# Kernel optimization log

Hardware: AMD Instinct MI355X
Metric: run time of the kernel (lower is better)

Reference implementation:

```python
import jax, jax.numpy as jnp
import numpy as np

WS = 7  # window size
NH = 8  # num heads


def _relative_position_index(ws):
    coords = np.stack(np.meshgrid(np.arange(ws), np.arange(ws), indexing='ij'), axis=0)
    flat = coords.reshape(2, -1)                       # [2, ws*ws]
    rel = flat[:, :, None] - flat[:, None, :]          # [2, N, N]
    rel = rel.transpose(1, 2, 0)                       # [N, N, 2]
    xx = (rel[:, :, 0] + ws - 1) * (2 * ws - 1)
    yy = rel[:, :, 1] + ws - 1
    return jnp.asarray(xx + yy, dtype=jnp.int32)       # [N, N]


def setup_inputs() -> dict:
    key = jax.random.key(0)
    ks = jax.random.split(key, 6)
    B_, N, C = 4096, WS * WS, 256
    return {
        'x': jax.random.normal(ks[0], (B_, N, C), dtype=jnp.float32),
        'qkv_w': jax.random.normal(ks[1], (C, 3 * C), dtype=jnp.float32) * 0.02,
        'qkv_b': jax.random.normal(ks[2], (3 * C,), dtype=jnp.float32) * 0.02,
        'rpb_table': jax.random.normal(ks[3], ((2 * WS - 1) ** 2, NH), dtype=jnp.float32) * 0.02,
        'proj_w': jax.random.normal(ks[4], (C, C), dtype=jnp.float32) * 0.02,
        'proj_b': jax.random.normal(ks[5], (C,), dtype=jnp.float32) * 0.02,
    }


def reference(x, qkv_w, qkv_b, rpb_table, proj_w, proj_b):
    B_, N, C = x.shape
    D = C // NH
    scale = D ** -0.5
    rpi = _relative_position_index(WS)                  # [N, N] int

    qkv = x @ qkv_w + qkv_b                             # [B, N, 3C]
    qkv = qkv.reshape(B_, N, 3, NH, D).transpose(2, 0, 3, 1, 4)
    q, k, v = qkv[0], qkv[1], qkv[2]                    # each [B, H, N, D]

    attn = jnp.einsum('bhnd,bhmd->bhnm', q * scale, k)  # [B, H, N, N]
    bias = rpb_table[rpi.reshape(-1)].reshape(N, N, NH).transpose(2, 0, 1)
    attn = jax.nn.softmax(attn + bias[None], axis=-1)

    out = jnp.einsum('bhnm,bhmd->bhnd', attn, v)        # [B, H, N, D]
    out = out.transpose(0, 2, 1, 3).reshape(B_, N, C)
    return out @ proj_w + proj_b
```

## Files before the change

### kernel.cpp

```cpp
#include <hip/hip_runtime.h>
#include <stdint.h>


typedef __attribute__((ext_vector_type(8))) short bf16x8;
typedef __attribute__((ext_vector_type(4))) float f32x4;

__device__ __forceinline__ unsigned short f2bf(float f) {
    unsigned u = __float_as_uint(f);
    u += 0x7fffu + ((u >> 16) & 1u);
    return (unsigned short)(u >> 16);
}
__device__ __forceinline__ unsigned pk2(float a, float b) {
    return (unsigned)f2bf(a) | ((unsigned)f2bf(b) << 16);
}

__global__ void k_prep(const float* __restrict__ qkv_w, const float* __restrict__ proj_w,
                       short* __restrict__ Wqkv_t, short* __restrict__ Wproj_t) {
    int tid = blockIdx.x * 256 + threadIdx.x;
    if (tid < 196608) {
        int nn = tid >> 8, kk = tid & 255;
        Wqkv_t[tid] = (short)f2bf(qkv_w[kk * 768 + nn]);
    } else {
        int t2 = tid - 196608;
        int nn = t2 >> 8, kk = t2 & 255;
        Wproj_t[t2] = (short)f2bf(proj_w[kk * 256 + nn]);
    }
}

#define XS_OFF 0
#define QS_OFF 16384
#define KS_OFF 32768
#define VT_OFF 49152
#define PL_OFF 67584

__global__ __launch_bounds__(512, 1) void k_fused(
        const float* __restrict__ x, const short* __restrict__ Wq,
        const short* __restrict__ Wp, const float* __restrict__ qkv_b,
        const float* __restrict__ rpb, const float* __restrict__ proj_b,
        float* __restrict__ out) {
    __shared__ __align__(16) short smem[76800];
    __shared__ float rpbs[1352];

    const int b = blockIdx.x;
    const int t = threadIdx.x;
    const int w = t >> 6, lane = t & 63;
    const int l15 = lane & 15, g = lane >> 4;
    const int cs8 = (l15 >> 1) & 3;
    const int swz = (g ^ cs8) << 3;

    f32x4 zero = {0.f, 0.f, 0.f, 0.f};

    for (int i = t; i < 1352; i += 512) rpbs[i] = rpb[i];
    #pragma unroll
    for (int i = 0; i < 4; i++) {
        int cid = t + i * 512;
        int tok = cid >> 5, c = cid & 31;
        uint4 w4 = make_uint4(0u, 0u, 0u, 0u);
        if (tok < 49) {
            const float4* s = (const float4*)(x + ((size_t)b * 49 + tok) * 256 + c * 8);
            float4 f0 = s[0], f1 = s[1];
            w4 = make_uint4(pk2(f0.x, f0.y), pk2(f0.z, f0.w),
                            pk2(f1.x, f1.y), pk2(f1.z, f1.w));
        }
        *(uint4*)&smem[XS_OFF + tok * 256 + ((c ^ (tok & 7)) << 3)] = w4;
    }
    __syncthreads();

    {
        f32x4 acc[6][4];
        #pragma unroll
        for (int i = 0; i < 6; i++)
            #pragma unroll
            for (int j = 0; j < 4; j++) acc[i][j] = zero;

        const short* wbase = Wq + (size_t)(w * 32 + l15) * 256 + g * 8;
        #pragma unroll
        for (int ks = 0; ks < 8; ks++) {
            bf16x8 af[6], bfj[4];
            #pragma unroll
            for (int p = 0; p < 3; p++)
                #pragma unroll
                for (int it = 0; it < 2; it++)
                    af[p * 2 + it] = *(const bf16x8*)(wbase + p * 65536 + it * 4096 + ks * 32);
            int xsl = (((ks << 2) + g) ^ (l15 & 7)) << 3;
            #pragma unroll
            for (int j = 0; j < 4; j++)
                bfj[j] = *(const bf16x8*)&smem[XS_OFF + (j * 16 + l15) * 256 + xsl];
            #pragma unroll
            for (int i = 0; i < 6; i++)
                #pragma unroll
                for (int j = 0; j < 4; j++)
                    acc[i][j] = __builtin_amdgcn_mfma_f32_16x16x32_bf16(
                        af[i], bfj[j], acc[i][j], 0, 0, 0);
        }
        #pragma unroll
        for (int p = 0; p < 2; p++) {
            int base = (p ? KS_OFF : QS_OFF) + w * 2048;
            #pragma unroll
            for (int it = 0; it < 2; it++) {
                int d0 = it * 16 + g * 4;
                float4 bv = *(const float4*)&qkv_b[p * 256 + w * 32 + d0];
                #pragma unroll
                for (int j = 0; j < 4; j++) {
                    int tok = j * 16 + l15;
                    f32x4 a = acc[p * 2 + it][j];
                    unsigned* dst = (unsigned*)&smem[base + tok * 32 +
                                                     (((d0 >> 3) ^ cs8) << 3) + (d0 & 7)];
                    dst[0] = pk2(a[0] + bv.x, a[1] + bv.y);
                    dst[1] = pk2(a[2] + bv.z, a[3] + bv.w);
                }
            }
        }
        {
            short* vt = &smem[VT_OFF + w * 2304];
            #pragma unroll
            for (int it = 0; it < 2; it++) {
                int d0 = it * 16 + g * 4;
                float4 bv = *(const float4*)&qkv_b[512 + w * 32 + d0];
                #pragma unroll
                for (int j = 0; j < 4; j++) {
                    int tok = j * 16 + l15;
                    f32x4 a = acc[4 + it][j];
                    vt[(d0 + 0) * 72 + tok] = (short)f2bf(a[0] + bv.x);
                    vt[(d0 + 1) * 72 + tok] = (short)f2bf(a[1] + bv.y);
                    vt[(d0 + 2) * 72 + tok] = (short)f2bf(a[2] + bv.z);
                    vt[(d0 + 3) * 72 + tok] = (short)f2bf(a[3] + bv.w);
                }
            }
        }
    }

    {
        const int h = w;
        const short* Kb = &smem[KS_OFF + h * 2048];
        const short* Qb = &smem[QS_OFF + h * 2048];
        bf16x8 ka[4], qb4[4], va[2][2];
        #pragma unroll
        for (int mt = 0; mt < 4; mt++)
            ka[mt] = *(const bf16x8*)&Kb[(mt * 16 + l15) * 32 + swz];
        #pragma unroll
        for (int nt = 0; nt < 4; nt++)
            qb4[nt] = *(const bf16x8*)&Qb[(nt * 16 + l15) * 32 + swz];
        #pragma unroll
        for (int dt = 0; dt < 2; dt++)
            #pragma unroll
            for (int kk = 0; kk < 2; kk++)
                va[dt][kk] = *(const bf16x8*)&smem[VT_OFF + h * 2304 +
                                                  (dt * 16 + l15) * 72 + kk * 32 + g * 8];
        short* Plw = &smem[PL_OFF + w * 1152];
        short* AOw = &smem[QS_OFF + h * 2048];
        const float scale = 0.17677669529663687f;

        #pragma unroll
        for (int nt = 0; nt < 4; nt++) {
            f32x4 s4[4];
            #pragma unroll
            for (int mt = 0; mt < 4; mt++)
                s4[mt] = __builtin_amdgcn_mfma_f32_16x16x32_bf16(ka[mt], qb4[nt], zero, 0, 0, 0);
            int n = nt * 16 + l15;
            int ni = n / 7;
            int an = 13 * ni + (n - 7 * ni) + 84;
            #pragma unroll
            for (int mt = 0; mt < 4; mt++)
                #pragma unroll
                for (int r = 0; r < 4; r++) {
                    int m = mt * 16 + g * 4 + r;
                    int mi = m / 7;
                    int idx = an - (13 * mi + (m - 7 * mi));
                    idx = idx < 0 ? 0 : (idx > 168 ? 168 : idx);
                    float val = s4[mt][r] * scale + rpbs[idx * 8 + h];
                    s4[mt][r] = (m < 49) ? val : -1e30f;
                }
            float tmax = -1e30f;
            #pragma unroll
            for (int mt = 0; mt < 4; mt++)
                #pragma unroll
                for (int r = 0; r < 4; r++) tmax = fmaxf(tmax, s4[mt][r]);
            tmax = fmaxf(tmax, __shfl_xor(tmax, 16));
            tmax = fmaxf(tmax, __shfl_xor(tmax, 32));
            float rsum = 0.f;
            #pragma unroll
            for (int mt = 0; mt < 4; mt++)
                #pragma unroll
                for (int r = 0; r < 4; r++) {
                    float e = __expf(s4[mt][r] - tmax);
                    s4[mt][r] = e;
                    rsum += e;
                }
            rsum += __shfl_xor(rsum, 16);
            rsum += __shfl_xor(rsum, 32);

            #pragma unroll
            for (int mt = 0; mt < 4; mt++) {
                unsigned* dst = (unsigned*)&Plw[l15 * 72 + mt * 16 + g * 4];
                dst[0] = pk2(s4[mt][0], s4[mt][1]);
                dst[1] = pk2(s4[mt][2], s4[mt][3]);
            }
            bf16x8 pb0 = *(const bf16x8*)&Plw[l15 * 72 + g * 8];
            bf16x8 pb1 = *(const bf16x8*)&Plw[l15 * 72 + 32 + g * 8];
            f32x4 o0 = __builtin_amdgcn_mfma_f32_16x16x32_bf16(va[0][0], pb0, zero, 0, 0, 0);
            o0 = __builtin_amdgcn_mfma_f32_16x16x32_bf16(va[0][1], pb1, o0, 0, 0, 0);
            f32x4 o1 = __builtin_amdgcn_mfma_f32_16x16x32_bf16(va[1][0], pb0, zero, 0, 0, 0);
            o1 = __builtin_amdgcn_mfma_f32_16x16x32_bf16(va[1][1], pb1, o1, 0, 0, 0);
            float inv = 1.f / rsum;
            {
                int d0 = g * 4;
                unsigned* dst = (unsigned*)&AOw[n * 32 + (((d0 >> 3) ^ cs8) << 3) + (d0 & 7)];
                dst[0] = pk2(o0[0] * inv, o0[1] * inv);
                dst[1] = pk2(o0[2] * inv, o0[3] * inv);
            }
            {
                int d0 = 16 + g * 4;
                unsigned* dst = (unsigned*)&AOw[n * 32 + (((d0 >> 3) ^ cs8) << 3) + (d0 & 7)];
                dst[0] = pk2(o1[0] * inv, o1[1] * inv);
                dst[1] = pk2(o1[2] * inv, o1[3] * inv);
            }
        }
    }
    __syncthreads();

    {
        f32x4 acc2[2][4];
        #pragma unroll
        for (int i = 0; i < 2; i++)
            #pragma unroll
            for (int j = 0; j < 4; j++) acc2[i][j] = zero;

        const short* pbase = Wp + (size_t)(w * 32 + l15) * 256 + g * 8;
        #pragma unroll
        for (int ks = 0; ks < 8; ks++) {
            bf16x8 af2[2], bf2[4];
            af2[0] = *(const bf16x8*)(pbase + ks * 32);
            af2[1] = *(const bf16x8*)(pbase + 4096 + ks * 32);
            #pragma unroll
            for (int j = 0; j < 4; j++)
                bf2[j] = *(const bf16x8*)&smem[QS_OFF + ks * 2048 + (j * 16 + l15) * 32 + swz];
            #pragma unroll
            for (int i = 0; i < 2; i++)
                #pragma unroll
                for (int j = 0; j < 4; j++)
                    acc2[i][j] = __builtin_amdgcn_mfma_f32_16x16x32_bf16(
                        af2[i], bf2[j], acc2[i][j], 0, 0, 0);
        }
        #pragma unroll
        for (int it = 0; it < 2; it++) {
            int fo = w * 32 + it * 16 + g * 4;
            float4 bv = *(const float4*)&proj_b[fo];
            #pragma unroll
            for (int j = 0; j < 4; j++) {
                int tok = j * 16 + l15;
                if (tok < 49) {
                    f32x4 a = acc2[it][j];
                    float4 val = make_float4(a[0] + bv.x, a[1] + bv.y,
                                             a[2] + bv.z, a[3] + bv.w);
                    *(float4*)&out[((size_t)b * 49 + tok) * 256 + fo] = val;
                }
            }
        }
    }
}

extern "C" void kernel_launch(void* const* d_in, const int* in_sizes, int n_in,
                              void* d_out, int out_size, void* d_ws, size_t ws_size,
                              hipStream_t stream) {
    const float* x      = (const float*)d_in[0];
    const float* qkv_w  = (const float*)d_in[1];
    const float* qkv_b  = (const float*)d_in[2];
    const float* rpb    = (const float*)d_in[3];
    const float* proj_w = (const float*)d_in[4];
    const float* proj_b = (const float*)d_in[5];
    float* out = (float*)d_out;

    short* Wqkv_t  = (short*)d_ws;
    short* Wproj_t = Wqkv_t + 768 * 256;
    if (ws_size < 524288ull) return;

    k_prep<<<1024, 256, 0, stream>>>(qkv_w, proj_w, Wqkv_t, Wproj_t);
    k_fused<<<4096, 512, 0, stream>>>(x, Wqkv_t, Wproj_t, qkv_b, rpb, proj_b, out);
}
```

Before: 679.9 us.

## Shrink shared memory via per-wave staging buffers to raise block occupancy

Replaces the separate Q, K, V-transpose and P shared-memory regions with one per-wave scratch area. Q, then K, then V are written into it one after another and loaded into registers, and the attention output reuses the x buffer. This cuts LDS use from about 153KB to about 70KB per block so more than one block can share a CU, and the launch bound now asks for 4 blocks per CU. The bias table is also transposed so each head reads its own contiguous slice. The cost is that the 96-float accumulator stays live into the attention phase, and the tighter launch bound caps registers. Together these raise the risk of heavy register spilling.

After: 1.130 ms. 66.2% more time.

```diff
diff --git a/kernel.cpp b/kernel.cpp
--- a/kernel.cpp
+++ b/kernel.cpp
@@ -28,17 +28,15 @@
 }
 
 #define XS_OFF 0
-#define QS_OFF 16384
-#define KS_OFF 32768
-#define VT_OFF 49152
-#define PL_OFF 67584
-
-__global__ __launch_bounds__(512, 1) void k_fused(
+#define AO_OFF 0
+#define SW_OFF 16384
+
+__global__ __launch_bounds__(512, 4) void k_fused(
         const float* __restrict__ x, const short* __restrict__ Wq,
         const short* __restrict__ Wp, const float* __restrict__ qkv_b,
         const float* __restrict__ rpb, const float* __restrict__ proj_b,
         float* __restrict__ out) {
-    __shared__ __align__(16) short smem[76800];
+    __shared__ __align__(16) short smem[34816];
     __shared__ float rpbs[1352];
 
     const int b = blockIdx.x;
@@ -50,7 +48,7 @@
 
     f32x4 zero = {0.f, 0.f, 0.f, 0.f};
 
-    for (int i = t; i < 1352; i += 512) rpbs[i] = rpb[i];
+    for (int i = t; i < 1352; i += 512) rpbs[(i & 7) * 169 + (i >> 3)] = rpb[i];
     #pragma unroll
     for (int i = 0; i < 4; i++) {
         int cid = t + i * 512;
@@ -66,13 +64,12 @@
     }
     __syncthreads();
 
+    f32x4 acc[6][4];
+    #pragma unroll
+    for (int i = 0; i < 6; i++)
+        #pragma unroll
+        for (int j = 0; j < 4; j++) acc[i][j] = zero;
     {
-        f32x4 acc[6][4];
-        #pragma unroll
-        for (int i = 0; i < 6; i++)
-            #pragma unroll
-            for (int j = 0; j < 4; j++) acc[i][j] = zero;
-
         const short* wbase = Wq + (size_t)(w * 32 + l15) * 256 + g * 8;
         #pragma unroll
         for (int ks = 0; ks < 8; ks++) {
@@ -93,62 +90,74 @@
                     acc[i][j] = __builtin_amdgcn_mfma_f32_16x16x32_bf16(
                         af[i], bfj[j], acc[i][j], 0, 0, 0);
         }
-        #pragma unroll
-        for (int p = 0; p < 2; p++) {
-            int base = (p ? KS_OFF : QS_OFF) + w * 2048;
-            #pragma unroll
-            for (int it = 0; it < 2; it++) {
-                int d0 = it * 16 + g * 4;
-                float4 bv = *(const float4*)&qkv_b[p * 256 + w * 32 + d0];
-                #pragma unroll
-                for (int j = 0; j < 4; j++) {
-                    int tok = j * 16 + l15;
-                    f32x4 a = acc[p * 2 + it][j];
-                    unsigned* dst = (unsigned*)&smem[base + tok * 32 +
-                                                     (((d0 >> 3) ^ cs8) << 3) + (d0 & 7)];
-                    dst[0] = pk2(a[0] + bv.x, a[1] + bv.y);
-                    dst[1] = pk2(a[2] + bv.z, a[3] + bv.w);
-                }
-            }
-        }
-        {
-            short* vt = &smem[VT_OFF + w * 2304];
-            #pragma unroll
-            for (int it = 0; it < 2; it++) {
-                int d0 = it * 16 + g * 4;
-                float4 bv = *(const float4*)&qkv_b[512 + w * 32 + d0];
-                #pragma unroll
-                for (int j = 0; j < 4; j++) {
-                    int tok = j * 16 + l15;
-                    f32x4 a = acc[4 + it][j];
-                    vt[(d0 + 0) * 72 + tok] = (short)f2bf(a[0] + bv.x);
-                    vt[(d0 + 1) * 72 + tok] = (short)f2bf(a[1] + bv.y);
-                    vt[(d0 + 2) * 72 + tok] = (short)f2bf(a[2] + bv.z);
-                    vt[(d0 + 3) * 72 + tok] = (short)f2bf(a[3] + bv.w);
-                }
-            }
-        }
-    }
+    }
+    __syncthreads();
 
     {
         const int h = w;
-        const short* Kb = &smem[KS_OFF + h * 2048];
-        const short* Qb = &smem[QS_OFF + h * 2048];
-        bf16x8 ka[4], qb4[4], va[2][2];
+        short* SW = &smem[SW_OFF + w * 2304];
+        const int d0a = g * 4;
+        const int d0b = 16 + g * 4;
+        const int sda = (((d0a >> 3) ^ cs8) << 3) + (d0a & 7);
+        const int sdb = (((d0b >> 3) ^ cs8) << 3) + (d0b & 7);
+
+        bf16x8 qb4[4], ka[4], va[2][2];
+
+        #pragma unroll
+        for (int it = 0; it < 2; it++) {
+            float4 bv = *(const float4*)&qkv_b[w * 32 + it * 16 + d0a];
+            int sd = it ? sdb : sda;
+            #pragma unroll
+            for (int j = 0; j < 4; j++) {
+                f32x4 a = acc[it][j];
+                unsigned* dst = (unsigned*)&SW[(j * 16 + l15) * 32 + sd];
+                dst[0] = pk2(a[0] + bv.x, a[1] + bv.y);
+                dst[1] = pk2(a[2] + bv.z, a[3] + bv.w);
+            }
+        }
+        #pragma unroll
+        for (int nt = 0; nt < 4; nt++)
+            qb4[nt] = *(const bf16x8*)&SW[(nt * 16 + l15) * 32 + swz];
+
+        #pragma unroll
+        for (int it = 0; it < 2; it++) {
+            float4 bv = *(const float4*)&qkv_b[256 + w * 32 + it * 16 + d0a];
+            int sd = it ? sdb : sda;
+            #pragma unroll
+            for (int j = 0; j < 4; j++) {
+                f32x4 a = acc[2 + it][j];
+                unsigned* dst = (unsigned*)&SW[(j * 16 + l15) * 32 + sd];
+                dst[0] = pk2(a[0] + bv.x, a[1] + bv.y);
+                dst[1] = pk2(a[2] + bv.z, a[3] + bv.w);
+            }
+        }
         #pragma unroll
         for (int mt = 0; mt < 4; mt++)
-            ka[mt] = *(const bf16x8*)&Kb[(mt * 16 + l15) * 32 + swz];
-        #pragma unroll
-        for (int nt = 0; nt < 4; nt++)
-            qb4[nt] = *(const bf16x8*)&Qb[(nt * 16 + l15) * 32 + swz];
+            ka[mt] = *(const bf16x8*)&SW[(mt * 16 + l15) * 32 + swz];
+
+        #pragma unroll
+        for (int it = 0; it < 2; it++) {
+            float4 bv = *(const float4*)&qkv_b[512 + w * 32 + it * 16 + d0a];
+            int d0 = it * 16 + d0a;
+            #pragma unroll
+            for (int j = 0; j < 4; j++) {
+                int tok = j * 16 + l15;
+                f32x4 a = acc[4 + it][j];
+                SW[(d0 + 0) * 72 + tok] = (short)f2bf(a[0] + bv.x);
+                SW[(d0 + 1) * 72 + tok] = (short)f2bf(a[1] + bv.y);
+                SW[(d0 + 2) * 72 + tok] = (short)f2bf(a[2] + bv.z);
+                SW[(d0 + 3) * 72 + tok] = (short)f2bf(a[3] + bv.w);
+            }
+        }
         #pragma unroll
         for (int dt = 0; dt < 2; dt++)
             #pragma unroll
             for (int kk = 0; kk < 2; kk++)
-                va[dt][kk] = *(const bf16x8*)&smem[VT_OFF + h * 2304 +
-                                                  (dt * 16 + l15) * 72 + kk * 32 + g * 8];
-        short* Plw = &smem[PL_OFF + w * 1152];
-        short* AOw = &smem[QS_OFF + h * 2048];
+                va[dt][kk] = *(const bf16x8*)&SW[(dt * 16 + l15) * 72 + kk * 32 + g * 8];
+
+        short* Plw = SW;
+        short* AOw = &smem[AO_OFF + h * 2048];
+        const float* rh = &rpbs[h * 169];
         const float scale = 0.17677669529663687f;
 
         #pragma unroll
@@ -168,7 +177,7 @@
                     int mi = m / 7;
                     int idx = an - (13 * mi + (m - 7 * mi));
                     idx = idx < 0 ? 0 : (idx > 168 ? 168 : idx);
-                    float val = s4[mt][r] * scale + rpbs[idx * 8 + h];
+                    float val = s4[mt][r] * scale + rh[idx];
                     s4[mt][r] = (m < 49) ? val : -1e30f;
                 }
             float tmax = -1e30f;
@@ -204,14 +213,12 @@
             o1 = __builtin_amdgcn_mfma_f32_16x16x32_bf16(va[1][1], pb1, o1, 0, 0, 0);
             float inv = 1.f / rsum;
             {
-                int d0 = g * 4;
-                unsigned* dst = (unsigned*)&AOw[n * 32 + (((d0 >> 3) ^ cs8) << 3) + (d0 & 7)];
+                unsigned* dst = (unsigned*)&AOw[n * 32 + sda];
                 dst[0] = pk2(o0[0] * inv, o0[1] * inv);
                 dst[1] = pk2(o0[2] * inv, o0[3] * inv);
             }
             {
-                int d0 = 16 + g * 4;
-                unsigned* dst = (unsigned*)&AOw[n * 32 + (((d0 >> 3) ^ cs8) << 3) + (d0 & 7)];
+                unsigned* dst = (unsigned*)&AOw[n * 32 + sdb];
                 dst[0] = pk2(o1[0] * inv, o1[1] * inv);
                 dst[1] = pk2(o1[2] * inv, o1[3] * inv);
             }
@@ -234,7 +241,7 @@
             af2[1] = *(const bf16x8*)(pbase + 4096 + ks * 32);
             #pragma unroll
             for (int j = 0; j < 4; j++)
-                bf2[j] = *(const bf16x8*)&smem[QS_OFF + ks * 2048 + (j * 16 + l15) * 32 + swz];
+                bf2[j] = *(const bf16x8*)&smem[AO_OFF + ks * 2048 + (j * 16 + l15) * 32 + swz];
             #pragma unroll
             for (int i = 0; i < 2; i++)
                 #pragma unroll
```
